# Kernel optimization log

Measured on AMD Instinct MI355X. Metric: run time of the kernel, lower is better.

Reference implementation:

```python
import jax, jax.numpy as jnp
import numpy as np

B = 1024
E = 200          # entity_dim (== relation_dim)
R = 200          # relation_dim
NE = 50000       # num_entities
NR = 400         # num_relations
OC = 32          # out_channels
FW = 9           # filt_w (filt_h = 1)
WP = E - FW + 1  # conv output width = 192
FC_IN = OC * WP  # 6144
EPS = 1e-5


def setup_inputs() -> dict:
    key = jax.random.key(0)
    ks = jax.random.split(key, 20)
    s = lambda n: 1.0 / np.sqrt(n)
    inp = {
        "e_s": jax.random.randint(ks[0], (B,), 0, NE, dtype=jnp.int32),
        "q_s": jax.random.randint(ks[1], (B,), 0, NR, dtype=jnp.int32),
        "e_c": jax.random.randint(ks[2], (B,), 0, NE, dtype=jnp.int32),
        "entity_emb": jax.random.normal(ks[3], (NE, E), jnp.float32) * 0.1,
        "relation_emb": jax.random.normal(ks[4], (NR, R), jnp.float32) * 0.1,
        "W1_w": jax.random.normal(ks[5], (E + R, R), jnp.float32) * s(E + R),
        "W1_b": jnp.zeros((R,), jnp.float32),
        "fc1_w": jax.random.normal(ks[6], (R, OC * FW), jnp.float32) * s(R),
        "fc1_b": jnp.zeros((OC * FW,), jnp.float32),
        "fc_w": jax.random.normal(ks[7], (FC_IN, E), jnp.float32) * s(FC_IN),
        "fc_b": jnp.zeros((E,), jnp.float32),
        "bn0_g": jnp.ones((1,), jnp.float32),
        "bn0_b": jnp.zeros((1,), jnp.float32),
        "bn0_m": jnp.zeros((1,), jnp.float32),
        "bn0_v": jnp.ones((1,), jnp.float32),
        "bn1_g": jnp.ones((OC,), jnp.float32),
        "bn1_b": jnp.zeros((OC,), jnp.float32),
        "bn1_m": jnp.zeros((OC,), jnp.float32),
        "bn1_v": jnp.ones((OC,), jnp.float32),
        "bn2_g": jnp.ones((E,), jnp.float32),
        "bn2_b": jnp.zeros((E,), jnp.float32),
        "bn2_m": jnp.zeros((E,), jnp.float32),
        "bn2_v": jnp.ones((E,), jnp.float32),
        "bias_b": jnp.zeros((NE,), jnp.float32),
    }
    return inp


def reference(e_s, q_s, e_c, entity_emb, relation_emb, W1_w, W1_b,
              fc1_w, fc1_b, fc_w, fc_b,
              bn0_g, bn0_b, bn0_m, bn0_v,
              bn1_g, bn1_b, bn1_m, bn1_v,
              bn2_g, bn2_b, bn2_m, bn2_v, bias_b):
    es = entity_emb[e_s]                      # [B,E]
    ec = entity_emb[e_c]                      # [B,E]
    r = relation_emb[q_s]                     # [B,R]
    # W1: Linear(E+R -> R); here R == E so e1 has width E
    e1 = jnp.concatenate([es, ec], -1) @ W1_w + W1_b          # [B,E]
    # bn0: single channel, inference mode
    x = (e1 - bn0_m) * (bn0_g / jnp.sqrt(bn0_v + EPS)) + bn0_b  # [B,E]
    # per-sample dynamic filters from fc1(r)
    k = (r @ fc1_w + fc1_b).reshape(B, OC, FW)                # [B,OC,FW]
    # grouped conv (groups=B) == per-sample 1D sliding dot products
    patches = jnp.stack([x[:, w:w + WP] for w in range(FW)], axis=-1)  # [B,WP,FW]
    conv = jnp.einsum('bpw,bow->bop', patches, k)             # [B,OC,WP]
    # bn1 over the OC channel, inference mode
    conv = (conv - bn1_m[:, None]) * (bn1_g / jnp.sqrt(bn1_v + EPS))[:, None] + bn1_b[:, None]
    flat = conv.reshape(B, FC_IN)                             # [B, OC*WP]
    h = flat @ fc_w + fc_b                                    # [B,E]
    h = (h - bn2_m) * (bn2_g / jnp.sqrt(bn2_v + EPS)) + bn2_b
    h = jax.nn.relu(h)
    logits = h @ entity_emb.T + bias_b                        # [B,NE]
    return jax.nn.sigmoid(logits)
```

## Files before the change

### kernel.cpp

```cpp
#include <hip/hip_runtime.h>

#define B_   1024
#define E_   200
#define NE_  50000
#define OC_  32
#define FW_  9
#define WP_  192
#define FCIN 6144
#define CATK 400
#define KDIM 288

typedef __attribute__((ext_vector_type(8))) short short8;
typedef __attribute__((ext_vector_type(4))) float floatx4;
typedef __attribute__((ext_vector_type(4))) unsigned short ushort4v;

static __device__ __forceinline__ float bf2f(unsigned short u) {
  return __uint_as_float(((unsigned)u) << 16);
}
static __device__ __forceinline__ unsigned short f2bf(float f) {
  unsigned u = __float_as_uint(f);
  u += 0x7FFFu + ((u >> 16) & 1u);
  return (unsigned short)(u >> 16);
}

__global__ __launch_bounds__(256) void k_cvt(
    const float* __restrict__ in, unsigned short* __restrict__ out, int n4) {
  int i = blockIdx.x * 256 + threadIdx.x;
  if (i >= n4) return;
  float4 v = ((const float4*)in)[i];
  ushort4v o = {f2bf(v.x), f2bf(v.y), f2bf(v.z), f2bf(v.w)};
  ((ushort4v*)out)[i] = o;
}

__global__ __launch_bounds__(256) void k_gather(
    const int* __restrict__ e_s, const int* __restrict__ q_s, const int* __restrict__ e_c,
    const float* __restrict__ ent, const float* __restrict__ rel,
    unsigned short* __restrict__ cat, unsigned short* __restrict__ rbuf) {
  int idx = blockIdx.x * 256 + threadIdx.x;
  if (idx < B_ * CATK) {
    int s = idx / CATK, i = idx - s * CATK;
    int row = (i < E_) ? e_s[s] : e_c[s];
    int col = (i < E_) ? i : i - E_;
    cat[idx] = f2bf(ent[row * E_ + col]);
  } else {
    int j = idx - B_ * CATK;
    if (j < B_ * E_) {
      int s = j / E_, i = j - s * E_;
      rbuf[j] = f2bf(rel[q_s[s] * E_ + i]);
    }
  }
}

__global__ __launch_bounds__(256) void k_transpose_lds(
    const float* __restrict__ in, unsigned short* __restrict__ out,
    int N, int Npad, int K) {
  __shared__ unsigned short lds[64][65];
  int n0 = blockIdx.x * 64, k0 = blockIdx.y * 64;
  int tx = threadIdx.x & 63, ty = threadIdx.x >> 6;
#pragma unroll
  for (int kk = 0; kk < 16; kk++) {
    int k = k0 + ty + 4 * kk;
    int n = n0 + tx;
    unsigned short v = 0;
    if (k < K && n < N) v = f2bf(in[(long)k * N + n]);
    lds[ty + 4 * kk][tx] = v;
  }
  __syncthreads();
#pragma unroll
  for (int kk = 0; kk < 16; kk++) {
    int k = k0 + tx;
    int n = n0 + ty + 4 * kk;
    if (n < Npad && k < K) out[(long)n * K + k] = lds[tx][ty + 4 * kk];
  }
}

template<int NK, int RQ>
static __device__ __forceinline__ floatx4 gemm_64x16(
    const unsigned short* __restrict__ A, int lda,
    const unsigned short* __restrict__ Bt, int ldb, int m0, int n0) {
  int lane = threadIdx.x & 63;
  int wv   = threadIdx.x >> 6;
  int l16  = lane & 15, quad = lane >> 4;
  const unsigned short* ap = A  + (long)(m0 + 16 * wv + l16) * lda + quad * 8;
  const unsigned short* bp = Bt + (long)(n0 + l16) * ldb + quad * 8;
  floatx4 acc = {0.f, 0.f, 0.f, 0.f};
#pragma unroll 4
  for (int ks = 0; ks < NK; ks++) {
    short8 a = *(const short8*)(ap + ks * 32);
    short8 b = *(const short8*)(bp + ks * 32);
    acc = __builtin_amdgcn_mfma_f32_16x16x32_bf16(a, b, acc, 0, 0, 0);
  }
  if (RQ > 0) {
    short8 z = {0,0,0,0,0,0,0,0};
    short8 a = (quad < RQ) ? *(const short8*)(ap + NK * 32) : z;
    short8 b = (quad < RQ) ? *(const short8*)(bp + NK * 32) : z;
    acc = __builtin_amdgcn_mfma_f32_16x16x32_bf16(a, b, acc, 0, 0, 0);
  }
  return acc;
}

__global__ __launch_bounds__(256) void k_gemm_e1(
    const unsigned short* __restrict__ cat, const unsigned short* __restrict__ W1T,
    const float* __restrict__ W1b,
    const float* __restrict__ g0, const float* __restrict__ b0,
    const float* __restrict__ m0p, const float* __restrict__ v0,
    unsigned short* __restrict__ xbuf) {
  int m0 = blockIdx.x * 64, n0 = blockIdx.y * 16;
  floatx4 acc = gemm_64x16<12, 2>(cat, CATK, W1T, CATK, m0, n0);
  int lane = threadIdx.x & 63, wv = threadIdx.x >> 6;
  int l16 = lane & 15, quad = lane >> 4;
  int j = n0 + l16;
  if (j < E_) {
    float s0  = g0[0] * rsqrtf(v0[0] + 1e-5f);
    float off = (W1b[j] - m0p[0]) * s0 + b0[0];
    int rbase = m0 + 16 * wv + quad * 4;
#pragma unroll
    for (int i = 0; i < 4; i++)
      xbuf[(rbase + i) * E_ + j] = f2bf(acc[i] * s0 + off);
  }
}

__global__ __launch_bounds__(256) void k_gemm_k(
    const unsigned short* __restrict__ rbuf, const unsigned short* __restrict__ fc1T,
    const float* __restrict__ fc1b,
    const float* __restrict__ g1, const float* __restrict__ v1,
    unsigned short* __restrict__ kbuf) {
  int m0 = blockIdx.x * 64, n0 = blockIdx.y * 16;
  floatx4 acc = gemm_64x16<6, 1>(rbuf, E_, fc1T, E_, m0, n0);
  int lane = threadIdx.x & 63, wv = threadIdx.x >> 6;
  int l16 = lane & 15, quad = lane >> 4;
  int c = n0 + l16;
  int o = c / FW_;
  float s1 = g1[o] * rsqrtf(v1[o] + 1e-5f);
  float fb = fc1b[c];
  int rbase = m0 + 16 * wv + quad * 4;
#pragma unroll
  for (int i = 0; i < 4; i++)
    kbuf[(rbase + i) * KDIM + c] = f2bf((acc[i] + fb) * s1);
}

__global__ __launch_bounds__(256) void k_conv(
    const unsigned short* __restrict__ xbuf, const unsigned short* __restrict__ kbuf,
    const float* __restrict__ g1, const float* __restrict__ b1,
    const float* __restrict__ m1, const float* __restrict__ v1,
    unsigned short* __restrict__ flat) {
  __shared__ float xs[E_];
  __shared__ float ks[KDIM];
  __shared__ float beta[OC_];
  int b = blockIdx.x, tid = threadIdx.x;
  if (tid < E_)  xs[tid] = bf2f(xbuf[b * E_ + tid]);
  for (int i = tid; i < KDIM; i += 256) ks[i] = bf2f(kbuf[b * KDIM + i]);
  if (tid < OC_) {
    float s = g1[tid] * rsqrtf(v1[tid] + 1e-5f);
    beta[tid] = b1[tid] - m1[tid] * s;
  }
  __syncthreads();
#pragma unroll
  for (int u = 0; u < FCIN / 256; u++) {
    int t = u * 256 + tid;
    int o = t / WP_, p = t - o * WP_;
    float acc = beta[o];
#pragma unroll
    for (int w = 0; w < FW_; w++) acc += xs[p + w] * ks[o * FW_ + w];
    flat[b * FCIN + t] = f2bf(acc);
  }
}

__global__ __launch_bounds__(256) void k_gemm_fc(
    const unsigned short* __restrict__ flat, const unsigned short* __restrict__ fcwT,
    float* __restrict__ partial) {
  int m0 = blockIdx.x * 64, n0 = blockIdx.y * 16, kc = blockIdx.z;
  int lane = threadIdx.x & 63, wv = threadIdx.x >> 6;
  int l16 = lane & 15, quad = lane >> 4;
  const unsigned short* ap = flat + (long)(m0 + 16 * wv + l16) * FCIN + kc * 768 + quad * 8;
  const unsigned short* bp = fcwT + (long)(n0 + l16) * FCIN + kc * 768 + quad * 8;
  floatx4 acc = {0.f, 0.f, 0.f, 0.f};
#pragma unroll 4
  for (int ks = 0; ks < 24; ks++) {
    short8 a = *(const short8*)(ap + ks * 32);
    short8 b = *(const short8*)(bp + ks * 32);
    acc = __builtin_amdgcn_mfma_f32_16x16x32_bf16(a, b, acc, 0, 0, 0);
  }
  int j = n0 + l16;
  int rbase = m0 + 16 * wv + quad * 4;
#pragma unroll
  for (int i = 0; i < 4; i++)
    partial[((long)kc * B_ + rbase + i) * 208 + j] = acc[i];
}

__global__ __launch_bounds__(256) void k_fc_epi(
    const float* __restrict__ partial, const float* __restrict__ fcb,
    const float* __restrict__ g2, const float* __restrict__ b2,
    const float* __restrict__ m2, const float* __restrict__ v2,
    unsigned short* __restrict__ hbuf) {
  int idx = blockIdx.x * 256 + threadIdx.x;
  if (idx >= B_ * E_) return;
  int m = idx / E_, j = idx - m * E_;
  float s = 0.f;
#pragma unroll
  for (int kc = 0; kc < 8; kc++) s += partial[((long)kc * B_ + m) * 208 + j];
  float s2 = g2[j] * rsqrtf(v2[j] + 1e-5f);
  float h = (s + fcb[j] - m2[j]) * s2 + b2[j];
  hbuf[idx] = f2bf(fmaxf(h, 0.f));
}

__global__ __launch_bounds__(512, 4) void k_gemm_out(
    const unsigned short* __restrict__ hbuf, const unsigned short* __restrict__ entb,
    const float* __restrict__ bias, float* __restrict__ out) {
  __shared__ __align__(16) unsigned short Blds[7 * 4 * 128 * 8];
  int g = blockIdx.x;
  int xcd = g & 7, local_ = g >> 3;
  int T = (xcd < 4 ? xcd * 196 : 784 + (xcd - 4) * 195) + local_;
  int mt = T & 3, nt = T >> 2;
  int m0 = mt * 256, n0 = nt * 128;
  int tid = threadIdx.x;

#pragma unroll
  for (int it = 0; it < 7; ++it) {
    int idx = it * 512 + tid;
    int ks = idx >> 9, qd = (idx >> 7) & 3, np = idx & 127;
    int col = 8 * (np & 15) + (np >> 4);
    int n = n0 + col;
    int kb = ks * 32 + qd * 8;
    short8 v = {0, 0, 0, 0, 0, 0, 0, 0};
    if (kb < 200 && n < NE_) v = *(const short8*)(entb + (long)n * E_ + kb);
    *(short8*)(Blds + idx * 8) = v;
  }
  __syncthreads();

  int lane = tid & 63, wv = tid >> 6;
  int l16 = lane & 15, quad = lane >> 4;
  const unsigned short* ap0 = hbuf + (long)(m0 + wv * 32 + l16) * E_ + quad * 8;
  const unsigned short* ap1 = ap0 + 16 * E_;

  floatx4 acc[16];
#pragma unroll
  for (int i = 0; i < 16; ++i) acc[i] = (floatx4){0.f, 0.f, 0.f, 0.f};

#pragma unroll
  for (int ks = 0; ks < 6; ++ks) {
    short8 a0 = *(const short8*)(ap0 + ks * 32);
    short8 a1 = *(const short8*)(ap1 + ks * 32);
    const unsigned short* bb = Blds + (ks * 4 + quad) * 1024 + l16 * 8;
#pragma unroll
    for (int nf = 0; nf < 8; ++nf) {
      short8 b = *(const short8*)(bb + nf * 128);
      acc[nf]     = __builtin_amdgcn_mfma_f32_16x16x32_bf16(a0, b, acc[nf], 0, 0, 0);
      acc[8 + nf] = __builtin_amdgcn_mfma_f32_16x16x32_bf16(a1, b, acc[8 + nf], 0, 0, 0);
    }
  }
  {
    short8 z = {0, 0, 0, 0, 0, 0, 0, 0};
    short8 a0 = (quad == 0) ? *(const short8*)(ap0 + 192) : z;
    short8 a1 = (quad == 0) ? *(const short8*)(ap1 + 192) : z;
    const unsigned short* bb = Blds + (24 + quad) * 1024 + l16 * 8;
#pragma unroll
    for (int nf = 0; nf < 8; ++nf) {
      short8 b = *(const short8*)(bb + nf * 128);
      acc[nf]     = __builtin_amdgcn_mfma_f32_16x16x32_bf16(a0, b, acc[nf], 0, 0, 0);
      acc[8 + nf] = __builtin_amdgcn_mfma_f32_16x16x32_bf16(a1, b, acc[8 + nf], 0, 0, 0);
    }
  }

  int nb = n0 + 8 * l16;
  if (nb >= NE_) return;
  float4 bi0 = *(const float4*)(bias + nb);
  float4 bi1 = *(const float4*)(bias + nb + 4);
#pragma unroll
  for (int mf = 0; mf < 2; ++mf) {
#pragma unroll
    for (int i = 0; i < 4; ++i) {
      int row = m0 + wv * 32 + mf * 16 + quad * 4 + i;
      float4 v0, v1;
      v0.x = 1.f / (1.f + __expf(-(acc[mf * 8 + 0][i] + bi0.x)));
      v0.y = 1.f / (1.f + __expf(-(acc[mf * 8 + 1][i] + bi0.y)));
      v0.z = 1.f / (1.f + __expf(-(acc[mf * 8 + 2][i] + bi0.z)));
      v0.w = 1.f / (1.f + __expf(-(acc[mf * 8 + 3][i] + bi0.w)));
      v1.x = 1.f / (1.f + __expf(-(acc[mf * 8 + 4][i] + bi1.x)));
      v1.y = 1.f / (1.f + __expf(-(acc[mf * 8 + 5][i] + bi1.y)));
      v1.z = 1.f / (1.f + __expf(-(acc[mf * 8 + 6][i] + bi1.z)));
      v1.w = 1.f / (1.f + __expf(-(acc[mf * 8 + 7][i] + bi1.w)));
      float* op = out + (long)row * NE_ + nb;
      *(float4*)op = v0;
      *(float4*)(op + 4) = v1;
    }
  }
}

extern "C" void kernel_launch(void* const* d_in, const int* in_sizes, int n_in,
                              void* d_out, int out_size, void* d_ws, size_t ws_size,
                              hipStream_t stream) {
  const int* e_s = (const int*)d_in[0];
  const int* q_s = (const int*)d_in[1];
  const int* e_c = (const int*)d_in[2];
  const float* ent  = (const float*)d_in[3];
  const float* rel  = (const float*)d_in[4];
  const float* W1w  = (const float*)d_in[5];
  const float* W1b  = (const float*)d_in[6];
  const float* fc1w = (const float*)d_in[7];
  const float* fc1b = (const float*)d_in[8];
  const float* fcw  = (const float*)d_in[9];
  const float* fcb  = (const float*)d_in[10];
  const float* g0 = (const float*)d_in[11];
  const float* b0 = (const float*)d_in[12];
  const float* m0 = (const float*)d_in[13];
  const float* v0 = (const float*)d_in[14];
  const float* g1 = (const float*)d_in[15];
  const float* b1 = (const float*)d_in[16];
  const float* m1 = (const float*)d_in[17];
  const float* v1 = (const float*)d_in[18];
  const float* g2 = (const float*)d_in[19];
  const float* b2 = (const float*)d_in[20];
  const float* m2 = (const float*)d_in[21];
  const float* v2 = (const float*)d_in[22];
  const float* bias = (const float*)d_in[23];
  float* out = (float*)d_out;

  char* w = (char*)d_ws;
  unsigned short* entb = (unsigned short*)(w + 0);
  unsigned short* cat  = (unsigned short*)(w + 20000256);
  unsigned short* rbuf = (unsigned short*)(w + 20819712);
  unsigned short* W1T  = (unsigned short*)(w + 21229568);
  unsigned short* fc1T = (unsigned short*)(w + 21396224);
  unsigned short* fcwT = (unsigned short*)(w + 21511680);
  unsigned short* xbuf = (unsigned short*)(w + 24067840);
  unsigned short* kbuf = (unsigned short*)(w + 24477696);
  unsigned short* flat = (unsigned short*)(w + 25067776);
  unsigned short* hbuf = (unsigned short*)(w + 37650944);
  float* partial       = (float*)(w + 38060800);

  k_cvt<<<dim3((NE_ * E_ / 4 + 255) / 256), dim3(256), 0, stream>>>(ent, entb, NE_ * E_ / 4);
  k_gather<<<dim3((B_ * CATK + B_ * E_) / 256), dim3(256), 0, stream>>>(
      e_s, q_s, e_c, ent, rel, cat, rbuf);
  k_transpose_lds<<<dim3(4, 7),  dim3(256), 0, stream>>>(W1w,  W1T,  200, 208, CATK);
  k_transpose_lds<<<dim3(5, 4),  dim3(256), 0, stream>>>(fc1w, fc1T, 288, 288, E_);
  k_transpose_lds<<<dim3(4, 96), dim3(256), 0, stream>>>(fcw,  fcwT, 200, 208, FCIN);

  k_gemm_e1<<<dim3(16, 13), dim3(256), 0, stream>>>(cat, W1T, W1b, g0, b0, m0, v0, xbuf);
  k_gemm_k<<<dim3(16, 18), dim3(256), 0, stream>>>(rbuf, fc1T, fc1b, g1, v1, kbuf);
  k_conv<<<dim3(B_), dim3(256), 0, stream>>>(xbuf, kbuf, g1, b1, m1, v1, flat);
  k_gemm_fc<<<dim3(16, 13, 8), dim3(256), 0, stream>>>(flat, fcwT, partial);
  k_fc_epi<<<dim3((B_ * E_ + 255) / 256), dim3(256), 0, stream>>>(
      partial, fcb, g2, b2, m2, v2, hbuf);
  k_gemm_out<<<dim3(1564), dim3(512), 0, stream>>>(hbuf, entb, bias, out);
}
```

Measured before the change: 426.0 us.

## Merge prep kernels and small GEMMs into single launches; register-block the conv

Five preprocessing launches (entity conversion, gather, three weight transposes) become one kernel that dispatches on block index ranges. The two small GEMMs (e1 and the dynamic filter k) likewise share one launch. The per-sample conv now gives each thread one channel and a 24-wide strip, keeps the 9 filter taps and a window of x in registers, and writes packed pairs of bf16 outputs. The aim is to cut launch overhead and gaps between small kernels and reduce LDS traffic in the conv, at the cost of more complex block dispatch and higher register use.

```diff
diff --git a/kernel.cpp b/kernel.cpp
--- a/kernel.cpp
+++ b/kernel.cpp
@@ -23,39 +23,22 @@
   return (unsigned short)(u >> 16);
 }
 
-__global__ __launch_bounds__(256) void k_cvt(
-    const float* __restrict__ in, unsigned short* __restrict__ out, int n4) {
-  int i = blockIdx.x * 256 + threadIdx.x;
-  if (i >= n4) return;
-  float4 v = ((const float4*)in)[i];
-  ushort4v o = {f2bf(v.x), f2bf(v.y), f2bf(v.z), f2bf(v.w)};
-  ((ushort4v*)out)[i] = o;
-}
-
-__global__ __launch_bounds__(256) void k_gather(
-    const int* __restrict__ e_s, const int* __restrict__ q_s, const int* __restrict__ e_c,
-    const float* __restrict__ ent, const float* __restrict__ rel,
-    unsigned short* __restrict__ cat, unsigned short* __restrict__ rbuf) {
-  int idx = blockIdx.x * 256 + threadIdx.x;
-  if (idx < B_ * CATK) {
-    int s = idx / CATK, i = idx - s * CATK;
-    int row = (i < E_) ? e_s[s] : e_c[s];
-    int col = (i < E_) ? i : i - E_;
-    cat[idx] = f2bf(ent[row * E_ + col]);
-  } else {
-    int j = idx - B_ * CATK;
-    if (j < B_ * E_) {
-      int s = j / E_, i = j - s * E_;
-      rbuf[j] = f2bf(rel[q_s[s] * E_ + i]);
-    }
-  }
-}
-
-__global__ __launch_bounds__(256) void k_transpose_lds(
+#define PREP_CVT_BLKS   9766
+#define PREP_GATH_BLKS  2400
+#define PREP_W1_BLKS    28
+#define PREP_FC1_BLKS   20
+#define PREP_FCW_BLKS   384
+#define PREP_R1 (PREP_CVT_BLKS)
+#define PREP_R2 (PREP_R1 + PREP_GATH_BLKS)
+#define PREP_R3 (PREP_R2 + PREP_W1_BLKS)
+#define PREP_R4 (PREP_R3 + PREP_FC1_BLKS)
+#define PREP_TOTAL (PREP_R4 + PREP_FCW_BLKS)
+
+static __device__ __forceinline__ void transpose_region(
     const float* __restrict__ in, unsigned short* __restrict__ out,
-    int N, int Npad, int K) {
-  __shared__ unsigned short lds[64][65];
-  int n0 = blockIdx.x * 64, k0 = blockIdx.y * 64;
+    int N, int Npad, int K, int bx, int by,
+    unsigned short (*lds)[65]) {
+  int n0 = bx * 64, k0 = by * 64;
   int tx = threadIdx.x & 63, ty = threadIdx.x >> 6;
 #pragma unroll
   for (int kk = 0; kk < 16; kk++) {
@@ -71,6 +54,46 @@
     int k = k0 + tx;
     int n = n0 + ty + 4 * kk;
     if (n < Npad && k < K) out[(long)n * K + k] = lds[tx][ty + 4 * kk];
+  }
+}
+
+__global__ __launch_bounds__(256) void k_prep(
+    const float* __restrict__ ent, const float* __restrict__ rel,
+    const int* __restrict__ e_s, const int* __restrict__ q_s, const int* __restrict__ e_c,
+    const float* __restrict__ W1w, const float* __restrict__ fc1w, const float* __restrict__ fcw,
+    unsigned short* __restrict__ entb, unsigned short* __restrict__ cat,
+    unsigned short* __restrict__ rbuf, unsigned short* __restrict__ W1T,
+    unsigned short* __restrict__ fc1T, unsigned short* __restrict__ fcwT) {
+  __shared__ unsigned short lds[64][65];
+  int blk = blockIdx.x, tid = threadIdx.x;
+  if (blk < PREP_R1) {
+    int i = blk * 256 + tid;
+    if (i < NE_ * E_ / 4) {
+      float4 v = ((const float4*)ent)[i];
+      ushort4v o = {f2bf(v.x), f2bf(v.y), f2bf(v.z), f2bf(v.w)};
+      ((ushort4v*)entb)[i] = o;
+    }
+  } else if (blk < PREP_R2) {
+    int idx = (blk - PREP_R1) * 256 + tid;
+    if (idx < B_ * CATK) {
+      int s = idx / CATK, i = idx - s * CATK;
+      int row = (i < E_) ? e_s[s] : e_c[s];
+      int col = (i < E_) ? i : i - E_;
+      cat[idx] = f2bf(ent[row * E_ + col]);
+    } else {
+      int j = idx - B_ * CATK;
+      int s = j / E_, i = j - s * E_;
+      rbuf[j] = f2bf(rel[q_s[s] * E_ + i]);
+    }
+  } else if (blk < PREP_R3) {
+    int l = blk - PREP_R2;
+    transpose_region(W1w, W1T, 200, 208, CATK, l % 4, l / 4, lds);
+  } else if (blk < PREP_R4) {
+    int l = blk - PREP_R3;
+    transpose_region(fc1w, fc1T, 288, 288, E_, l % 5, l / 5, lds);
+  } else {
+    int l = blk - PREP_R4;
+    transpose_region(fcw, fcwT, 200, 208, FCIN, l % 4, l / 4, lds);
   }
 }
 
@@ -99,44 +122,44 @@
   return acc;
 }
 
-__global__ __launch_bounds__(256) void k_gemm_e1(
+__global__ __launch_bounds__(256) void k_gemm_ek(
     const unsigned short* __restrict__ cat, const unsigned short* __restrict__ W1T,
     const float* __restrict__ W1b,
     const float* __restrict__ g0, const float* __restrict__ b0,
     const float* __restrict__ m0p, const float* __restrict__ v0,
-    unsigned short* __restrict__ xbuf) {
-  int m0 = blockIdx.x * 64, n0 = blockIdx.y * 16;
-  floatx4 acc = gemm_64x16<12, 2>(cat, CATK, W1T, CATK, m0, n0);
-  int lane = threadIdx.x & 63, wv = threadIdx.x >> 6;
-  int l16 = lane & 15, quad = lane >> 4;
-  int j = n0 + l16;
-  if (j < E_) {
-    float s0  = g0[0] * rsqrtf(v0[0] + 1e-5f);
-    float off = (W1b[j] - m0p[0]) * s0 + b0[0];
-    int rbase = m0 + 16 * wv + quad * 4;
-#pragma unroll
-    for (int i = 0; i < 4; i++)
-      xbuf[(rbase + i) * E_ + j] = f2bf(acc[i] * s0 + off);
-  }
-}
-
-__global__ __launch_bounds__(256) void k_gemm_k(
+    unsigned short* __restrict__ xbuf,
     const unsigned short* __restrict__ rbuf, const unsigned short* __restrict__ fc1T,
     const float* __restrict__ fc1b,
     const float* __restrict__ g1, const float* __restrict__ v1,
     unsigned short* __restrict__ kbuf) {
-  int m0 = blockIdx.x * 64, n0 = blockIdx.y * 16;
-  floatx4 acc = gemm_64x16<6, 1>(rbuf, E_, fc1T, E_, m0, n0);
+  int blk = blockIdx.x;
   int lane = threadIdx.x & 63, wv = threadIdx.x >> 6;
   int l16 = lane & 15, quad = lane >> 4;
-  int c = n0 + l16;
-  int o = c / FW_;
-  float s1 = g1[o] * rsqrtf(v1[o] + 1e-5f);
-  float fb = fc1b[c];
-  int rbase = m0 + 16 * wv + quad * 4;
-#pragma unroll
-  for (int i = 0; i < 4; i++)
-    kbuf[(rbase + i) * KDIM + c] = f2bf((acc[i] + fb) * s1);
+  if (blk < 208) {
+    int m0 = (blk & 15) * 64, n0 = (blk >> 4) * 16;
+    floatx4 acc = gemm_64x16<12, 2>(cat, CATK, W1T, CATK, m0, n0);
+    int j = n0 + l16;
+    if (j < E_) {
+      float s0  = g0[0] * rsqrtf(v0[0] + 1e-5f);
+      float off = (W1b[j] - m0p[0]) * s0 + b0[0];
+      int rbase = m0 + 16 * wv + quad * 4;
+#pragma unroll
+      for (int i = 0; i < 4; i++)
+        xbuf[(rbase + i) * E_ + j] = f2bf(acc[i] * s0 + off);
+    }
+  } else {
+    int l = blk - 208;
+    int m0 = (l & 15) * 64, n0 = (l >> 4) * 16;
+    floatx4 acc = gemm_64x16<6, 1>(rbuf, E_, fc1T, E_, m0, n0);
+    int c = n0 + l16;
+    int o = c / FW_;
+    float s1 = g1[o] * rsqrtf(v1[o] + 1e-5f);
+    float fb = fc1b[c];
+    int rbase = m0 + 16 * wv + quad * 4;
+#pragma unroll
+    for (int i = 0; i < 4; i++)
+      kbuf[(rbase + i) * KDIM + c] = f2bf((acc[i] + fb) * s1);
+  }
 }
 
 __global__ __launch_bounds__(256) void k_conv(
@@ -155,14 +178,29 @@
     beta[tid] = b1[tid] - m1[tid] * s;
   }
   __syncthreads();
-#pragma unroll
-  for (int u = 0; u < FCIN / 256; u++) {
-    int t = u * 256 + tid;
-    int o = t / WP_, p = t - o * WP_;
-    float acc = beta[o];
-#pragma unroll
-    for (int w = 0; w < FW_; w++) acc += xs[p + w] * ks[o * FW_ + w];
-    flat[b * FCIN + t] = f2bf(acc);
+  int o = tid >> 3, pc = tid & 7;
+  int p0 = pc * 24;
+  float kw[FW_];
+#pragma unroll
+  for (int w = 0; w < FW_; w++) kw[w] = ks[o * FW_ + w];
+  float xw[32];
+#pragma unroll
+  for (int q = 0; q < 8; q++) {
+    float4 v = *(const float4*)&xs[p0 + 4 * q];
+    xw[4 * q + 0] = v.x; xw[4 * q + 1] = v.y; xw[4 * q + 2] = v.z; xw[4 * q + 3] = v.w;
+  }
+  float bo = beta[o];
+  unsigned short* fp = flat + b * FCIN + o * WP_ + p0;
+#pragma unroll
+  for (int j = 0; j < 24; j += 2) {
+    float a0 = bo, a1 = bo;
+#pragma unroll
+    for (int w = 0; w < FW_; w++) {
+      a0 += xw[j + w] * kw[w];
+      a1 += xw[j + 1 + w] * kw[w];
+    }
+    unsigned pack = (unsigned)f2bf(a0) | ((unsigned)f2bf(a1) << 16);
+    *(unsigned*)(fp + j) = pack;
   }
 }
 
@@ -329,15 +367,10 @@
   unsigned short* hbuf = (unsigned short*)(w + 37650944);
   float* partial       = (float*)(w + 38060800);
 
-  k_cvt<<<dim3((NE_ * E_ / 4 + 255) / 256), dim3(256), 0, stream>>>(ent, entb, NE_ * E_ / 4);
-  k_gather<<<dim3((B_ * CATK + B_ * E_) / 256), dim3(256), 0, stream>>>(
-      e_s, q_s, e_c, ent, rel, cat, rbuf);
-  k_transpose_lds<<<dim3(4, 7),  dim3(256), 0, stream>>>(W1w,  W1T,  200, 208, CATK);
-  k_transpose_lds<<<dim3(5, 4),  dim3(256), 0, stream>>>(fc1w, fc1T, 288, 288, E_);
-  k_transpose_lds<<<dim3(4, 96), dim3(256), 0, stream>>>(fcw,  fcwT, 200, 208, FCIN);
-
-  k_gemm_e1<<<dim3(16, 13), dim3(256), 0, stream>>>(cat, W1T, W1b, g0, b0, m0, v0, xbuf);
-  k_gemm_k<<<dim3(16, 18), dim3(256), 0, stream>>>(rbuf, fc1T, fc1b, g1, v1, kbuf);
+  k_prep<<<dim3(PREP_TOTAL), dim3(256), 0, stream>>>(
+      ent, rel, e_s, q_s, e_c, W1w, fc1w, fcw, entb, cat, rbuf, W1T, fc1T, fcwT);
+  k_gemm_ek<<<dim3(496), dim3(256), 0, stream>>>(
+      cat, W1T, W1b, g0, b0, m0, v0, xbuf, rbuf, fc1T, fc1b, g1, v1, kbuf);
   k_conv<<<dim3(B_), dim3(256), 0, stream>>>(xbuf, kbuf, g1, b1, m1, v1, flat);
   k_gemm_fc<<<dim3(16, 13, 8), dim3(256), 0, stream>>>(flat, fcwT, partial);
   k_fc_epi<<<dim3((B_ * E_ + 255) / 256), dim3(256), 0, stream>>>(
```

Result: faster. 392.3 us (-7.9%).
